# Kernel optimization log

Hardware: AMD Instinct MI355X
Metric: run time of the kernel (lower is better)

Reference implementation:

```python
import jax, jax.numpy as jnp
import numpy as np

S, B, D, N, DH = 2048, 2, 1024, 16, 64  # seq, batch, d_model, n_head, d_head
LN_EPS = 1e-5


def setup_inputs() -> dict:
    key = jax.random.key(0)
    ks = jax.random.split(key, 8)
    h = jax.random.normal(ks[0], (S, B, D), dtype=jnp.float32)
    Wq = jax.random.normal(ks[1], (D, N * DH), dtype=jnp.float32) * 0.02
    Wkv = jax.random.normal(ks[2], (D, 2 * N * DH), dtype=jnp.float32) * 0.02
    Wo = jax.random.normal(ks[3], (N * DH, D), dtype=jnp.float32) * 0.02
    ln_gamma = jnp.ones((D,), dtype=jnp.float32)
    ln_beta = jnp.zeros((D,), dtype=jnp.float32)
    # persistent compressive-memory state from a previous segment
    memory = jax.random.normal(ks[4], (B, N, DH, DH), dtype=jnp.float32)
    # normalization is a sum of (elu(k)+1) over ~S positions -> strictly positive, O(S)
    mem_norm = jax.random.uniform(ks[5], (B, 1, N, DH), dtype=jnp.float32) * S + 1.0
    gate_beta = jnp.ones((1,), dtype=jnp.float32) * 0.01  # beta_eps
    return {"h": h, "Wq": Wq, "Wkv": Wkv, "Wo": Wo, "ln_gamma": ln_gamma,
            "ln_beta": ln_beta, "memory": memory, "mem_norm": mem_norm,
            "gate_beta": gate_beta}


def reference(h, Wq, Wkv, Wo, ln_gamma, ln_beta, memory, mem_norm, gate_beta):
    scale = 1.0 / np.sqrt(DH).astype(np.float32)
    # projections (pre_lnorm=False, mems=None -> c == h)
    q = (h @ Wq).reshape(S, B, N, DH)
    k, v = jnp.split(h @ Wkv, 2, axis=-1)
    k = k.reshape(S, B, N, DH)
    v = v.reshape(S, B, N, DH)
    # local quadratic attention
    score = jnp.einsum('ibnd,jbnd->ijbn', q, k) * scale  # [S,S,B,N]
    prob = jax.nn.softmax(score, axis=1)
    attn_vec = jnp.einsum('ijbn,jbnd->ibnd', prob, v).reshape(S, B, N * DH)
    # memory retrieval (NOTE: source swaps K/V in the _update_memory call;
    # it is done under no_grad -> stop_gradient here)
    cached_Q = jax.nn.elu(q.swapaxes(0, 1)) + 1.0          # [B,S,N,DH]
    num = jnp.einsum('bsnk,bnkv->bsnv', cached_Q, memory)   # [B,S,N,DH]
    den = jnp.einsum('bsnk,bvnk->bsnv', cached_Q, mem_norm)  # [B,S,N,1]
    content_A = jax.lax.stop_gradient(num / den)            # [B,S,N,DH]
    # gated injection
    g = jax.nn.sigmoid(gate_beta)                           # [1]
    inj = g * content_A.swapaxes(0, 1).reshape(S, B, N * DH) + (1.0 - g) * attn_vec
    attn_out = inj @ Wo
    # post layernorm residual
    y = h + attn_out
    mu = jnp.mean(y, axis=-1, keepdims=True)
    var = jnp.mean((y - mu) ** 2, axis=-1, keepdims=True)
    return (y - mu) / jnp.sqrt(var + LN_EPS) * ln_gamma + ln_beta
```

## Files before the change

### kernel.cpp

```cpp
#include <hip/hip_runtime.h>


typedef unsigned short ushort_t;
typedef unsigned int uint32;

typedef __bf16 bf16x8 __attribute__((ext_vector_type(8)));
typedef float f32x4 __attribute__((ext_vector_type(4)));
typedef float f32x16 __attribute__((ext_vector_type(16)));
typedef unsigned short u16x8 __attribute__((ext_vector_type(8)));
typedef unsigned short u16x4 __attribute__((ext_vector_type(4)));
typedef unsigned int u32x4 __attribute__((ext_vector_type(4)));

typedef const __attribute__((address_space(1))) void gvoid_t;
typedef __attribute__((address_space(3))) void lvoid_t;

#define S_LEN 2048
#define BATCH 2
#define NHEAD 16

__device__ __forceinline__ ushort_t f2bf(float x) {
  union { float f; unsigned u; } c; c.f = x;
  unsigned r = (c.u + 0x7FFFu + ((c.u >> 16) & 1u)) >> 16;
  return (ushort_t)r;
}
__device__ __forceinline__ float bf2f(ushort_t v) {
  union { unsigned u; float f; } c; c.u = ((unsigned)v) << 16;
  return c.f;
}

__global__ __launch_bounds__(256) void k_cvt_all(const float* __restrict__ h,
                                                 const float* __restrict__ Wq,
                                                 const float* __restrict__ Wkv,
                                                 const float* __restrict__ Wo,
                                                 ushort_t* __restrict__ hb,
                                                 ushort_t* __restrict__ wT,
                                                 ushort_t* __restrict__ woT) {
  const int z = blockIdx.z;
  if (z == 3) {
    int idx = (blockIdx.y * 64 + blockIdx.x) * 256 + threadIdx.x;
#pragma unroll
    for (int i = 0; i < 2; ++i) {
      int e = idx + i * 524288;
      float4 v = ((const float4*)h)[e];
      u16x4 o; o[0] = f2bf(v.x); o[1] = f2bf(v.y); o[2] = f2bf(v.z); o[3] = f2bf(v.w);
      ((u16x4*)hb)[e] = o;
    }
    return;
  }
  const float* W;
  ushort_t* WT;
  int N;
  if (z == 0)      { W = Wq;  WT = wT;                        N = 1024; }
  else if (z == 1) { W = Wkv; WT = wT + (size_t)1024 * 1024;  N = 2048; }
  else             { W = Wo;  WT = woT;                       N = 1024; }
  const int K = 1024;
  if (blockIdx.x * 32 >= N) return;
  __shared__ float tile[32][33];
  const int n0 = blockIdx.x * 32, k0 = blockIdx.y * 32;
  const int tx = threadIdx.x & 31, ty = threadIdx.x >> 5;
#pragma unroll
  for (int r = 0; r < 32; r += 8)
    tile[ty + r][tx] = W[(size_t)(k0 + ty + r) * N + n0 + tx];
  __syncthreads();
#pragma unroll
  for (int r = 0; r < 32; r += 8)
    WT[(size_t)(n0 + ty + r) * K + k0 + tx] = f2bf(tile[tx][ty + r]);
}

template <int OUT_BF16>
__global__ __launch_bounds__(256) void k_gemm_bt(const ushort_t* __restrict__ A,
                                                 const ushort_t* __restrict__ B,
                                                 void* __restrict__ Cv, int M, int N, int K,
                                                 int nbx) {
  __shared__ __attribute__((aligned(16))) ushort_t As[128 * 64];
  __shared__ __attribute__((aligned(16))) ushort_t Bs[128 * 64];
  const int per = gridDim.x >> 3;
  const int fl = (blockIdx.x & 7) * per + (blockIdx.x >> 3);
  const int m0 = (fl / nbx) * 128, n0 = (fl % nbx) * 128;
  const int tid = threadIdx.x, w = tid >> 6, lane = tid & 63;
  const int wm = (w >> 1) * 64, wn = (w & 1) * 64;
  const int l15 = lane & 15, l4 = lane >> 4;
  const int sw = ((lane & 7) ^ (lane >> 3)) << 3;
  f32x4 acc[4][4];
#pragma unroll
  for (int i = 0; i < 4; ++i)
#pragma unroll
    for (int j = 0; j < 4; ++j)
#pragma unroll
      for (int r = 0; r < 4; ++r) acc[i][j][r] = 0.f;

  for (int k0 = 0; k0 < K; k0 += 64) {
    __syncthreads();
#pragma unroll
    for (int r = 0; r < 4; ++r) {
      int rowb = r * 32 + w * 8;
      const ushort_t* ga = A + (size_t)(m0 + rowb + (lane >> 3)) * K + k0 + sw;
      const ushort_t* gb = B + (size_t)(n0 + rowb + (lane >> 3)) * K + k0 + sw;
      __builtin_amdgcn_global_load_lds((gvoid_t*)ga, (lvoid_t*)(As + rowb * 64), 16, 0, 0);
      __builtin_amdgcn_global_load_lds((gvoid_t*)gb, (lvoid_t*)(Bs + rowb * 64), 16, 0, 0);
    }
    __syncthreads();
#pragma unroll
    for (int kk = 0; kk < 2; ++kk) {
      bf16x8 af[4], bfr[4];
#pragma unroll
      for (int i = 0; i < 4; ++i) {
        int row = wm + i * 16 + l15;
        af[i] = *(const bf16x8*)&As[row * 64 + (((kk * 4 + l4) ^ (row & 7)) << 3)];
      }
#pragma unroll
      for (int j = 0; j < 4; ++j) {
        int row = wn + j * 16 + l15;
        bfr[j] = *(const bf16x8*)&Bs[row * 64 + (((kk * 4 + l4) ^ (row & 7)) << 3)];
      }
#pragma unroll
      for (int i = 0; i < 4; ++i)
#pragma unroll
        for (int j = 0; j < 4; ++j)
          acc[i][j] = __builtin_amdgcn_mfma_f32_16x16x32_bf16(af[i], bfr[j], acc[i][j], 0, 0, 0);
    }
  }
#pragma unroll
  for (int i = 0; i < 4; ++i)
#pragma unroll
    for (int j = 0; j < 4; ++j)
#pragma unroll
      for (int r = 0; r < 4; ++r) {
        int row = m0 + wm + i * 16 + l4 * 4 + r;
        int col = n0 + wn + j * 16 + l15;
        if (OUT_BF16)
          ((ushort_t*)Cv)[(size_t)row * N + col] = f2bf(acc[i][j][r]);
        else
          ((float*)Cv)[(size_t)row * N + col] = acc[i][j][r];
      }
}

__global__ __launch_bounds__(256) void k_gemm64(const ushort_t* __restrict__ A,
                                                const ushort_t* __restrict__ B,
                                                ushort_t* __restrict__ C, int M, int N, int K,
                                                int nbx) {
  __shared__ __attribute__((aligned(16))) ushort_t As[64 * 64];
  __shared__ __attribute__((aligned(16))) ushort_t Bs[128 * 64];
  const int per = gridDim.x >> 3;
  const int fl = (blockIdx.x & 7) * per + (blockIdx.x >> 3);
  const int m0 = (fl / nbx) * 64, n0 = (fl % nbx) * 128;
  const int tid = threadIdx.x, w = tid >> 6, lane = tid & 63;
  const int wn = w * 32;
  const int l15 = lane & 15, l4 = lane >> 4;
  const int sw = ((lane & 7) ^ (lane >> 3)) << 3;
  f32x4 acc[4][2];
#pragma unroll
  for (int i = 0; i < 4; ++i)
#pragma unroll
    for (int j = 0; j < 2; ++j)
#pragma unroll
      for (int r = 0; r < 4; ++r) acc[i][j][r] = 0.f;

  for (int k0 = 0; k0 < K; k0 += 64) {
    __syncthreads();
#pragma unroll
    for (int r = 0; r < 2; ++r) {
      int rowb = w * 16 + r * 8;
      const ushort_t* ga = A + (size_t)(m0 + rowb + (lane >> 3)) * K + k0 + sw;
      __builtin_amdgcn_global_load_lds((gvoid_t*)ga, (lvoid_t*)(As + rowb * 64), 16, 0, 0);
    }
#pragma unroll
    for (int r = 0; r < 4; ++r) {
      int rowb = w * 32 + r * 8;
      const ushort_t* gb = B + (size_t)(n0 + rowb + (lane >> 3)) * K + k0 + sw;
      __builtin_amdgcn_global_load_lds((gvoid_t*)gb, (lvoid_t*)(Bs + rowb * 64), 16, 0, 0);
    }
    __syncthreads();
#pragma unroll
    for (int kk = 0; kk < 2; ++kk) {
      bf16x8 af[4], bfr[2];
#pragma unroll
      for (int i = 0; i < 4; ++i) {
        int row = i * 16 + l15;
        af[i] = *(const bf16x8*)&As[row * 64 + (((kk * 4 + l4) ^ (row & 7)) << 3)];
      }
#pragma unroll
      for (int j = 0; j < 2; ++j) {
        int row = wn + j * 16 + l15;
        bfr[j] = *(const bf16x8*)&Bs[row * 64 + (((kk * 4 + l4) ^ (row & 7)) << 3)];
      }
#pragma unroll
      for (int i = 0; i < 4; ++i)
#pragma unroll
        for (int j = 0; j < 2; ++j)
          acc[i][j] = __builtin_amdgcn_mfma_f32_16x16x32_bf16(af[i], bfr[j], acc[i][j], 0, 0, 0);
    }
  }
#pragma unroll
  for (int i = 0; i < 4; ++i)
#pragma unroll
    for (int j = 0; j < 2; ++j)
#pragma unroll
      for (int r = 0; r < 4; ++r)
        C[(size_t)(m0 + i * 16 + l4 * 4 + r) * N + n0 + wn + j * 16 + l15] = f2bf(acc[i][j][r]);
}

__global__ __launch_bounds__(256) void k_vt(const ushort_t* __restrict__ qkv,
                                            ushort_t* __restrict__ vt) {
  __shared__ uint32 tile[64 * 65];
  const int jt = blockIdx.x, bn = blockIdx.y, b = bn & 1, n = bn >> 1;
  const int tid = threadIdx.x;
  const int j0 = jt * 64;
#pragma unroll
  for (int rr = 0; rr < 2; ++rr) {
    int lin = rr * 2048 + tid * 8;
    int j = lin >> 6, d0 = lin & 63;
    u16x8 v = *(const u16x8*)(qkv + (size_t)(j0 + j) * 6144 + b * 3072 + 2048 + n * 64 + d0);
#pragma unroll
    for (int e = 0; e < 8; ++e) tile[j * 65 + d0 + e] = v[e];
  }
  __syncthreads();
#pragma unroll
  for (int rr = 0; rr < 2; ++rr) {
    int lin = rr * 2048 + tid * 8;
    int d = lin >> 6, jj = lin & 63;
    u16x8 o;
#pragma unroll
    for (int e = 0; e < 8; ++e) o[e] = (ushort_t)tile[(jj + e) * 65 + d];
    *(u16x8*)(vt + ((size_t)bn * 64 + d) * 2048 + j0 + jj) = o;
  }
}

__global__ __launch_bounds__(256, 4) void k_attn(const ushort_t* __restrict__ qkv,
                                                 const ushort_t* __restrict__ vt,
                                                 ushort_t* o0, ushort_t* o1,
                                                 float* __restrict__ l0,
                                                 float* __restrict__ l1) {
  __shared__ __attribute__((aligned(16))) ushort_t Ks[2][4096];
  __shared__ __attribute__((aligned(16))) ushort_t VTs[2][4096];
  const int bid = blockIdx.x;
  const int fl = (bid & 7) * 128 + (bid >> 3);
  const int qb = fl & 15, bn = (fl >> 4) & 31, z = fl >> 9;
  const int b = bn & 1, n = bn >> 1;
  const int tid = threadIdx.x, w = tid >> 6, lane = tid & 63;
  const int l31 = lane & 31, h = lane >> 5;
  const int qrow = qb * 128 + w * 32 + l31;
  const size_t qoff = (size_t)qrow * 6144 + b * 3072 + n * 64;
  const float CEXP = 0.18033688011113723f;
  bf16x8 qf[4];
#pragma unroll
  for (int ks = 0; ks < 4; ++ks) {
    u16x8 qv = *(const u16x8*)(qkv + qoff + ks * 16 + h * 8);
    union { u16x8 u; bf16x8 v; } cu;
#pragma unroll
    for (int e = 0; e < 8; ++e) cu.u[e] = f2bf(bf2f(qv[e]) * CEXP);
    qf[ks] = cu.v;
  }
  const int fA = (l31 & 7) ^ (l31 >> 3);
  const int fB = fA ^ 4;

  const int t0 = z * 16;
  const int sw0 = (((lane & 7) ^ (lane >> 3) ^ (w * 2)) & 7) << 3;
  const int sw1 = (((lane & 7) ^ (lane >> 3) ^ (w * 2 + 1)) & 7) << 3;
  const ushort_t* kp0 = qkv + (size_t)(t0 * 64 + w * 16 + (lane >> 3)) * 6144 + b * 3072 + n * 64 + 1024 + sw0;
  const ushort_t* kp1 = qkv + (size_t)(t0 * 64 + w * 16 + 8 + (lane >> 3)) * 6144 + b * 3072 + n * 64 + 1024 + sw1;
  const ushort_t* vp0 = vt + ((size_t)bn * 64 + w * 16 + (lane >> 3)) * 2048 + t0 * 64 + sw0;
  const ushort_t* vp1 = vt + ((size_t)bn * 64 + w * 16 + 8 + (lane >> 3)) * 2048 + t0 * 64 + sw1;
  const size_t KSTRIDE = (size_t)64 * 6144;

  __builtin_amdgcn_global_load_lds((gvoid_t*)kp0, (lvoid_t*)(Ks[0] + (w * 16) * 64), 16, 0, 0);
  __builtin_amdgcn_global_load_lds((gvoid_t*)kp1, (lvoid_t*)(Ks[0] + (w * 16 + 8) * 64), 16, 0, 0);
  __builtin_amdgcn_global_load_lds((gvoid_t*)vp0, (lvoid_t*)(VTs[0] + (w * 16) * 64), 16, 0, 0);
  __builtin_amdgcn_global_load_lds((gvoid_t*)vp1, (lvoid_t*)(VTs[0] + (w * 16 + 8) * 64), 16, 0, 0);
  kp0 += KSTRIDE; kp1 += KSTRIDE; vp0 += 64; vp1 += 64;
  __syncthreads();

  f32x16 oacc[2];
#pragma unroll
  for (int r = 0; r < 16; ++r) { oacc[0][r] = 0.f; oacc[1][r] = 0.f; }
  float lsum = 0.f;

  for (int t = 0; t < 16; ++t) {
    const ushort_t* Kb = Ks[t & 1];
    const ushort_t* Vb = VTs[t & 1];
    if (t < 15) {
      ushort_t* kw = Ks[(t + 1) & 1];
      ushort_t* vw = VTs[(t + 1) & 1];
      __builtin_amdgcn_global_load_lds((gvoid_t*)kp0, (lvoid_t*)(kw + (w * 16) * 64), 16, 0, 0);
      __builtin_amdgcn_global_load_lds((gvoid_t*)kp1, (lvoid_t*)(kw + (w * 16 + 8) * 64), 16, 0, 0);
      __builtin_amdgcn_global_load_lds((gvoid_t*)vp0, (lvoid_t*)(vw + (w * 16) * 64), 16, 0, 0);
      __builtin_amdgcn_global_load_lds((gvoid_t*)vp1, (lvoid_t*)(vw + (w * 16 + 8) * 64), 16, 0, 0);
      kp0 += KSTRIDE; kp1 += KSTRIDE; vp0 += 64; vp1 += 64;
    }
#pragma unroll
    for (int jb = 0; jb < 2; ++jb) {
      f32x16 sv;
#pragma unroll
      for (int r = 0; r < 16; ++r) sv[r] = 0.f;
      const int rb = (jb * 32 + l31) * 64;
      const int fj = jb ? fB : fA;
      __builtin_amdgcn_s_setprio(1);
#pragma unroll
      for (int ks = 0; ks < 4; ++ks) {
        bf16x8 kf = *(const bf16x8*)&Kb[rb + ((((ks << 1) | h) ^ fj) << 3)];
        sv = __builtin_amdgcn_mfma_f32_32x32x16_bf16(kf, qf[ks], sv, 0, 0, 0);
      }
      __builtin_amdgcn_s_setprio(0);
#pragma unroll
      for (int r = 0; r < 16; ++r) sv[r] = __builtin_amdgcn_exp2f(sv[r]);
#pragma unroll
      for (int ks2 = 0; ks2 < 2; ++ks2) {
        const int q0 = ks2 * 2;
        uint32 X0, X1, Y0, Y1;
        asm volatile("v_cvt_pk_bf16_f32 %0, %1, %2" : "=v"(X0) : "v"(sv[q0 * 4 + 0]), "v"(sv[q0 * 4 + 1]));
        asm volatile("v_cvt_pk_bf16_f32 %0, %1, %2" : "=v"(X1) : "v"(sv[q0 * 4 + 2]), "v"(sv[q0 * 4 + 3]));
        asm volatile("v_cvt_pk_bf16_f32 %0, %1, %2" : "=v"(Y0) : "v"(sv[(q0 + 1) * 4 + 0]), "v"(sv[(q0 + 1) * 4 + 1]));
        asm volatile("v_cvt_pk_bf16_f32 %0, %1, %2" : "=v"(Y1) : "v"(sv[(q0 + 1) * 4 + 2]), "v"(sv[(q0 + 1) * 4 + 3]));
        asm volatile("v_permlane32_swap_b32 %0, %1" : "+v"(X0), "+v"(Y0));
        asm volatile("v_permlane32_swap_b32 %0, %1" : "+v"(X1), "+v"(Y1));
        union { u32x4 u; bf16x8 v; } pf;
        pf.u[0] = X0; pf.u[1] = X1; pf.u[2] = Y0; pf.u[3] = Y1;
        const int c = ((jb * 2 + ks2) << 1) | h;
        bf16x8 vf0 = *(const bf16x8*)&Vb[l31 * 64 + ((c ^ fA) << 3)];
        bf16x8 vf1 = *(const bf16x8*)&Vb[(32 + l31) * 64 + ((c ^ fB) << 3)];
        __builtin_amdgcn_s_setprio(1);
        oacc[0] = __builtin_amdgcn_mfma_f32_32x32x16_bf16(vf0, pf.v, oacc[0], 0, 0, 0);
        oacc[1] = __builtin_amdgcn_mfma_f32_32x32x16_bf16(vf1, pf.v, oacc[1], 0, 0, 0);
        __builtin_amdgcn_s_setprio(0);
      }
      float ls[8];
#pragma unroll
      for (int r = 0; r < 8; ++r) ls[r] = sv[r] + sv[r + 8];
#pragma unroll
      for (int st = 4; st >= 1; st >>= 1)
#pragma unroll
        for (int r = 0; r < st; ++r) ls[r] += ls[r + st];
      lsum += ls[0];
    }
    if (t < 15) __syncthreads();
  }
  const float l_run = lsum + __shfl_xor(lsum, 32);

  ushort_t* op = (z == 0) ? (o0 + (size_t)qrow * 2048 + b * 1024 + n * 64)
                          : (o1 + (size_t)qrow * 6144 + b * 3072 + 2048 + n * 64);
#pragma unroll
  for (int db = 0; db < 2; ++db)
#pragma unroll
    for (int qq = 0; qq < 4; ++qq) {
      u16x4 st;
#pragma unroll
      for (int m = 0; m < 4; ++m) st[m] = f2bf(oacc[db][qq * 4 + m]);
      *(u16x4*)(op + db * 32 + qq * 8 + h * 4) = st;
    }
  if (h == 0) {
    float* lp = (z == 0) ? l0 : l1;
    lp[qrow * 32 + bn] = l_run;
  }
}

__global__ __launch_bounds__(256) void k_gate2(const ushort_t* __restrict__ qkv,
                                               const ushort_t* __restrict__ o0,
                                               const float* __restrict__ l0,
                                               const float* __restrict__ l1,
                                               const float* __restrict__ mem,
                                               const float* __restrict__ mnorm,
                                               const float* __restrict__ gbeta,
                                               ushort_t* __restrict__ inj) {
  const int bn = blockIdx.y, b = bn & 1, n = bn >> 1;
  const int tid = threadIdx.x, w = tid >> 6, lane = tid & 63;
  const int l31 = lane & 31, h = lane >> 5;
  const int qrow = blockIdx.x * 128 + w * 32 + l31;
  const size_t qoff = (size_t)qrow * 6144 + b * 3072 + n * 64;

  float den = 0.f;
  bf16x8 cqf[4];
  const float* nrm = mnorm + (size_t)(b * NHEAD + n) * 64;
#pragma unroll
  for (int ks = 0; ks < 4; ++ks) {
    u16x8 qv = *(const u16x8*)(qkv + qoff + ks * 16 + h * 8);
    union { u16x8 u; bf16x8 v; } cu;
#pragma unroll
    for (int e = 0; e < 8; ++e) {
      float x = bf2f(qv[e]);
      float c = (x > 0.f) ? (x + 1.f) : __builtin_amdgcn_exp2f(x * 1.4426950408889634f);
      cu.u[e] = f2bf(c);
      den += c * nrm[ks * 16 + h * 8 + e];
    }
    cqf[ks] = cu.v;
  }
  den += __shfl_xor(den, 32);

  const float* mb = mem + (size_t)(b * NHEAD + n) * 4096;
  f32x16 accv[2];
#pragma unroll
  for (int r = 0; r < 16; ++r) { accv[0][r] = 0.f; accv[1][r] = 0.f; }
#pragma unroll
  for (int db = 0; db < 2; ++db)
#pragma unroll
    for (int ks = 0; ks < 4; ++ks) {
      union { u16x8 u; bf16x8 v; } af;
#pragma unroll
      for (int e = 0; e < 8; ++e)
        af.u[e] = f2bf(mb[(size_t)(ks * 16 + h * 8 + e) * 64 + db * 32 + l31]);
      accv[db] = __builtin_amdgcn_mfma_f32_32x32x16_bf16(af.v, cqf[ks], accv[db], 0, 0, 0);
    }

  const float lsum = l0[qrow * 32 + bn] + l1[qrow * 32 + bn];
  float g = 1.f / (1.f + expf(-gbeta[0]));
  float rden = 1.f / den, invl = 1.f / lsum;
  const ushort_t* p0 = o0 + (size_t)qrow * 2048 + b * 1024 + n * 64;
  const ushort_t* p1 = qkv + (size_t)qrow * 6144 + b * 3072 + 2048 + n * 64;
  ushort_t* op = inj + (size_t)qrow * 2048 + b * 1024 + n * 64;
#pragma unroll
  for (int db = 0; db < 2; ++db)
#pragma unroll
    for (int qq = 0; qq < 4; ++qq) {
      const int off = db * 32 + qq * 8 + h * 4;
      u16x4 a0 = *(const u16x4*)(p0 + off);
      u16x4 a1 = *(const u16x4*)(p1 + off);
      u16x4 st;
#pragma unroll
      for (int m = 0; m < 4; ++m) {
        float av = (bf2f(a0[m]) + bf2f(a1[m])) * invl;
        float content = accv[db][qq * 4 + m] * rden;
        st[m] = f2bf(g * content + (1.f - g) * av);
      }
      *(u16x4*)(op + off) = st;
    }
}

__global__ __launch_bounds__(256) void k_ln(const float* __restrict__ h,
                                            const ushort_t* __restrict__ aob,
                                            const float* __restrict__ gam,
                                            const float* __restrict__ bet,
                                            float* __restrict__ out) {
  const int m = blockIdx.x, t = threadIdx.x;
  const int lane = t & 63, w = t >> 6;
  __shared__ float redS[4], redQ[4];
  const size_t base = (size_t)m * 1024;
  float4 hv = ((const float4*)(h + base))[t];
  u16x4 av4 = ((const u16x4*)(aob + base))[t];
  float y0 = hv.x + bf2f(av4[0]), y1 = hv.y + bf2f(av4[1]);
  float y2 = hv.z + bf2f(av4[2]), y3 = hv.w + bf2f(av4[3]);
  float s = y0 + y1 + y2 + y3;
  float sq = y0 * y0 + y1 * y1 + y2 * y2 + y3 * y3;
#pragma unroll
  for (int mk = 32; mk >= 1; mk >>= 1) { s += __shfl_xor(s, mk); sq += __shfl_xor(sq, mk); }
  if (lane == 0) { redS[w] = s; redQ[w] = sq; }
  __syncthreads();
  float Ssum = redS[0] + redS[1] + redS[2] + redS[3];
  float Qsum = redQ[0] + redQ[1] + redQ[2] + redQ[3];
  float mu = Ssum * (1.f / 1024.f);
  float var = Qsum * (1.f / 1024.f) - mu * mu;
  float rstd = rsqrtf(var + 1e-5f);
  float4 g = ((const float4*)gam)[t];
  float4 bt = ((const float4*)bet)[t];
  float4 o;
  o.x = (y0 - mu) * rstd * g.x + bt.x;
  o.y = (y1 - mu) * rstd * g.y + bt.y;
  o.z = (y2 - mu) * rstd * g.z + bt.z;
  o.w = (y3 - mu) * rstd * g.w + bt.w;
  ((float4*)(out + base))[t] = o;
}

extern "C" void kernel_launch(void* const* d_in, const int* in_sizes, int n_in,
                              void* d_out, int out_size, void* d_ws, size_t ws_size,
                              hipStream_t stream) {
  const float* h = (const float*)d_in[0];
  const float* Wq = (const float*)d_in[1];
  const float* Wkv = (const float*)d_in[2];
  const float* Wo = (const float*)d_in[3];
  const float* gam = (const float*)d_in[4];
  const float* bet = (const float*)d_in[5];
  const float* mem = (const float*)d_in[6];
  const float* mnorm = (const float*)d_in[7];
  const float* gbeta = (const float*)d_in[8];
  float* out = (float*)d_out;

  char* ws = (char*)d_ws;
  ushort_t* hb  = (ushort_t*)(ws);
  ushort_t* wT  = (ushort_t*)(ws + (size_t)(8u << 20));
  ushort_t* woT = (ushort_t*)(ws + (size_t)(14u << 20));
  ushort_t* qkv = (ushort_t*)(ws + (size_t)(16u << 20));
  ushort_t* aob = (ushort_t*)(ws + (size_t)(16u << 20));
  ushort_t* vtb = (ushort_t*)(ws + (size_t)(40u << 20));
  ushort_t* o0  = hb;
  float*    l0  = (float*)(ws + (size_t)(8u << 20));
  float*    l1  = (float*)(ws + (size_t)(8u << 20) + (1u << 18));
  ushort_t* inj = vtb;

  k_cvt_all<<<dim3(64, 32, 4), 256, 0, stream>>>(h, Wq, Wkv, Wo, hb, wT, woT);
  k_gemm_bt<1><<<768, 256, 0, stream>>>(hb, wT, (void*)qkv, 4096, 3072, 1024, 24);
  k_vt<<<dim3(32, 32), 256, 0, stream>>>(qkv, vtb);
  k_attn<<<1024, 256, 0, stream>>>(qkv, vtb, o0, qkv, l0, l1);
  k_gate2<<<dim3(16, 32), 256, 0, stream>>>(qkv, o0, l0, l1, mem, mnorm, gbeta, inj);
  k_gemm64<<<512, 256, 0, stream>>>(inj, woT, aob, 4096, 1024, 1024, 8);
  k_ln<<<4096, 256, 0, stream>>>(h, aob, gam, bet, out);
}
```

Measured before the change: 133.2 us.

## Fuse V transpose into QKV GEMM epilogue and drop separate transpose kernel

Output tiles of the QKV projection GEMM that belong to the V columns are now staged through shared memory with an XOR swizzle. They are written directly in the transposed per-(batch,head) layout that attention consumes. This removes the standalone k_vt kernel, along with its launch and its extra global read and write of the V block. In exchange, those GEMM blocks do an extra LDS round trip with strided 8-element gathers that may hit bank conflicts. V is also no longer written into the qkv buffer in its row-major form.

```diff
diff --git a/kernel.cpp b/kernel.cpp
--- a/kernel.cpp
+++ b/kernel.cpp
@@ -67,13 +67,14 @@
     WT[(size_t)(n0 + ty + r) * K + k0 + tx] = f2bf(tile[tx][ty + r]);
 }
 
-template <int OUT_BF16>
 __global__ __launch_bounds__(256) void k_gemm_bt(const ushort_t* __restrict__ A,
                                                  const ushort_t* __restrict__ B,
-                                                 void* __restrict__ Cv, int M, int N, int K,
-                                                 int nbx) {
-  __shared__ __attribute__((aligned(16))) ushort_t As[128 * 64];
-  __shared__ __attribute__((aligned(16))) ushort_t Bs[128 * 64];
+                                                 ushort_t* __restrict__ C,
+                                                 ushort_t* __restrict__ vt,
+                                                 int M, int N, int K, int nbx) {
+  __shared__ __attribute__((aligned(16))) ushort_t smem[16384];
+  ushort_t* As = smem;
+  ushort_t* Bs = smem + 8192;
   const int per = gridDim.x >> 3;
   const int fl = (blockIdx.x & 7) * per + (blockIdx.x >> 3);
   const int m0 = (fl / nbx) * 128, n0 = (fl % nbx) * 128;
@@ -120,19 +121,49 @@
           acc[i][j] = __builtin_amdgcn_mfma_f32_16x16x32_bf16(af[i], bfr[j], acc[i][j], 0, 0, 0);
     }
   }
-#pragma unroll
-  for (int i = 0; i < 4; ++i)
-#pragma unroll
-    for (int j = 0; j < 4; ++j)
-#pragma unroll
-      for (int r = 0; r < 4; ++r) {
-        int row = m0 + wm + i * 16 + l4 * 4 + r;
-        int col = n0 + wn + j * 16 + l15;
-        if (OUT_BF16)
-          ((ushort_t*)Cv)[(size_t)row * N + col] = f2bf(acc[i][j][r]);
-        else
-          ((float*)Cv)[(size_t)row * N + col] = acc[i][j][r];
-      }
+
+  if (n0 >= 2048) {
+    __syncthreads();
+#pragma unroll
+    for (int i = 0; i < 4; ++i)
+#pragma unroll
+      for (int j = 0; j < 4; ++j)
+#pragma unroll
+        for (int r = 0; r < 4; ++r) {
+          int rl = wm + i * 16 + l4 * 4 + r;
+          int cl = wn + j * 16 + l15;
+          smem[rl * 128 + (cl ^ ((rl & 7) << 3))] = f2bf(acc[i][j][r]);
+        }
+    __syncthreads();
+    const int vbase = n0 - 2048;
+    const int s0 = m0 >> 1;
+#pragma unroll
+    for (int q = 0; q < 8; ++q) {
+      int lin = q * 256 + tid;
+      int cl = lin >> 4, sub = lin & 15;
+      int bb = sub >> 3, s8 = (sub & 7) * 8;
+      u16x8 o;
+#pragma unroll
+      for (int e = 0; e < 8; ++e) {
+        int tok = (s8 + e) * 2 + bb;
+        o[e] = smem[tok * 128 + (cl ^ ((tok & 7) << 3))];
+      }
+      int vcol = vbase + cl;
+      int nn = vcol >> 6, dd = vcol & 63;
+      *(u16x8*)(vt + ((size_t)(nn * 2 + bb) * 64 + dd) * 2048 + s0 + s8) = o;
+    }
+  } else {
+#pragma unroll
+    for (int i = 0; i < 4; ++i)
+#pragma unroll
+      for (int j = 0; j < 4; ++j)
+#pragma unroll
+        for (int r = 0; r < 4; ++r) {
+          int row = m0 + wm + i * 16 + l4 * 4 + r;
+          int col = n0 + wn + j * 16 + l15;
+          C[(size_t)row * N + col] = f2bf(acc[i][j][r]);
+        }
+  }
 }
 
 __global__ __launch_bounds__(256) void k_gemm64(const ushort_t* __restrict__ A,
@@ -198,32 +229,6 @@
 #pragma unroll
       for (int r = 0; r < 4; ++r)
         C[(size_t)(m0 + i * 16 + l4 * 4 + r) * N + n0 + wn + j * 16 + l15] = f2bf(acc[i][j][r]);
-}
-
-__global__ __launch_bounds__(256) void k_vt(const ushort_t* __restrict__ qkv,
-                                            ushort_t* __restrict__ vt) {
-  __shared__ uint32 tile[64 * 65];
-  const int jt = blockIdx.x, bn = blockIdx.y, b = bn & 1, n = bn >> 1;
-  const int tid = threadIdx.x;
-  const int j0 = jt * 64;
-#pragma unroll
-  for (int rr = 0; rr < 2; ++rr) {
-    int lin = rr * 2048 + tid * 8;
-    int j = lin >> 6, d0 = lin & 63;
-    u16x8 v = *(const u16x8*)(qkv + (size_t)(j0 + j) * 6144 + b * 3072 + 2048 + n * 64 + d0);
-#pragma unroll
-    for (int e = 0; e < 8; ++e) tile[j * 65 + d0 + e] = v[e];
-  }
-  __syncthreads();
-#pragma unroll
-  for (int rr = 0; rr < 2; ++rr) {
-    int lin = rr * 2048 + tid * 8;
-    int d = lin >> 6, jj = lin & 63;
-    u16x8 o;
-#pragma unroll
-    for (int e = 0; e < 8; ++e) o[e] = (ushort_t)tile[(jj + e) * 65 + d];
-    *(u16x8*)(vt + ((size_t)bn * 64 + d) * 2048 + j0 + jj) = o;
-  }
 }
 
 __global__ __launch_bounds__(256, 4) void k_attn(const ushort_t* __restrict__ qkv,
@@ -485,8 +490,7 @@
   ushort_t* inj = vtb;
 
   k_cvt_all<<<dim3(64, 32, 4), 256, 0, stream>>>(h, Wq, Wkv, Wo, hb, wT, woT);
-  k_gemm_bt<1><<<768, 256, 0, stream>>>(hb, wT, (void*)qkv, 4096, 3072, 1024, 24);
-  k_vt<<<dim3(32, 32), 256, 0, stream>>>(qkv, vtb);
+  k_gemm_bt<<<768, 256, 0, stream>>>(hb, wT, qkv, vtb, 4096, 3072, 1024, 24);
   k_attn<<<1024, 256, 0, stream>>>(qkv, vtb, o0, qkv, l0, l1);
   k_gate2<<<dim3(16, 32), 256, 0, stream>>>(qkv, o0, l0, l1, mem, mnorm, gbeta, inj);
   k_gemm64<<<512, 256, 0, stream>>>(inj, woT, aob, 4096, 1024, 1024, 8);
```

After: 130.5 us. 2.0% less time.
